# Kernel tuning notes

Measured on AMD Instinct MI355X. Metric: run time of the kernel, lower is better.

## Reference

```python
import jax, jax.numpy as jnp
import numpy as np

HIDDEN = 100  # hard-coded in the torch module


def setup_inputs() -> dict:
    key = jax.random.key(0)
    k1, k2, k3, k4, k5 = jax.random.split(key, 5)
    dims, N, M = 32, 4096, 8192
    centroids = jax.random.normal(k1, (N, dims), dtype=jnp.float32)
    x = jax.random.normal(k2, (M, dims), dtype=jnp.float32)
    # torch Linear params: y = x @ W.T (+ b)
    W1 = jax.random.normal(k3, (HIDDEN, dims), dtype=jnp.float32) / np.sqrt(dims)
    W2 = jax.random.normal(k4, (dims, HIDDEN), dtype=jnp.float32) / np.sqrt(HIDDEN)
    b2 = jax.random.uniform(k5, (dims,), dtype=jnp.float32, minval=-0.1, maxval=0.1)
    return {"centroids": centroids, "x": x, "W1": W1, "W2": W2, "b2": b2}


def reference(centroids, x, W1, W2, b2):
    dims = centroids.shape[1]
    # small MLP: Linear(dims,100,no bias) -> Linear(100,dims) -> tanh, then gate by centroids
    loc = jnp.tanh((centroids @ W1.T) @ W2.T + b2) * centroids  # [N, dims]
    # covariance = eye(dims) * var(centroids) (scalar, unbiased var over all elements)
    var = jnp.var(centroids, ddof=1)
    # diagonal-Gaussian log_prob, pairwise [N, M] via ||x-loc||^2 expansion (no NxMxD cube)
    sq = (
        jnp.sum(x * x, axis=1)[None, :]
        + jnp.sum(loc * loc, axis=1)[:, None]
        - 2.0 * (loc @ x.T)
    )  # [N, M]
    log_norm = dims * jnp.log(2.0 * jnp.pi * var)
    logp = -0.5 * (sq / var + log_norm)  # [N, M]
    return jnp.exp(logp).T  # [M, N]
```

## Files before the change

kernel.cpp:

```cpp
#include <hip/hip_runtime.h>
#include <math.h>

#define DIMS 32
#define NROWS 4096
#define MROWS 8192
#define HID 100

#define L2E 1.44269504088896340736f

typedef float f32x4 __attribute__((ext_vector_type(4)));
typedef short bf16x8 __attribute__((ext_vector_type(8)));

__global__ __launch_bounds__(256) void k_init(const float* __restrict__ c,
                                              const float* __restrict__ W1,
                                              const float* __restrict__ W2,
                                              float* __restrict__ part,
                                              float* __restrict__ Mmat) {
    int b = blockIdx.x, t = threadIdx.x;
    const float4* c4 = (const float4*)c;
    float s = 0.0f, q = 0.0f;
    #pragma unroll
    for (int i = 0; i < 16; i++) {
        float4 a = c4[b * 4096 + i * 256 + t];
        s += a.x + a.y + a.z + a.w;
        q += a.x * a.x + a.y * a.y + a.z * a.z + a.w * a.w;
    }
    #pragma unroll
    for (int off = 32; off > 0; off >>= 1) {
        s += __shfl_down(s, off);
        q += __shfl_down(q, off);
    }
    __shared__ float red[8];
    int lane = t & 63, wid = t >> 6;
    if (lane == 0) { red[wid] = s; red[4 + wid] = q; }
    __syncthreads();
    if (t == 0) {
        part[2 * b]     = red[0] + red[1] + red[2] + red[3];
        part[2 * b + 1] = red[4] + red[5] + red[6] + red[7];
    }
    if (b == 0) {
        __shared__ float w1s[HID * DIMS];
        __shared__ float w2s[DIMS * HID];
        for (int i = t; i < HID * DIMS; i += 256) { w1s[i] = W1[i]; w2s[i] = W2[i]; }
        __syncthreads();
        #pragma unroll
        for (int o = 0; o < 4; o++) {
            int id = o * 256 + t;
            int r = id >> 5, cc = id & 31;
            float a = 0.0f;
            for (int j = 0; j < HID; j++) a += w2s[r * HID + j] * w1s[j * DIMS + cc];
            Mmat[id] = a;
        }
    }
}

__device__ __forceinline__ void load_var(const float* part, float& iv, float& var) {
    float S = 0.0f, Q = 0.0f;
    #pragma unroll
    for (int i = 0; i < 8; i++) { S += part[2 * i]; Q += part[2 * i + 1]; }
    const float cnt = (float)(NROWS * DIMS);
    var = (Q - S * S / cnt) / (cnt - 1.0f);
    iv = 1.0f / var;
}

__device__ __forceinline__ float tanh_fast(float x) {
    float xc = fminf(fmaxf(x, -10.0f), 10.0f);
    float e = __builtin_amdgcn_exp2f(xc * (2.0f * L2E));
    return (e - 1.0f) * __builtin_amdgcn_rcpf(e + 1.0f);
}

__device__ __forceinline__ unsigned short f2bf(float f) {
    unsigned int u = __float_as_uint(f);
    u += 0x7FFFu + ((u >> 16) & 1u);
    return (unsigned short)(u >> 16);
}

__global__ __launch_bounds__(256) void k_prep(const float* __restrict__ cent,
                                              const float* __restrict__ x,
                                              const float* __restrict__ b2,
                                              const float* __restrict__ part,
                                              const float* __restrict__ Mmat,
                                              float* __restrict__ A,
                                              float* __restrict__ B,
                                              unsigned short* __restrict__ xb,
                                              unsigned short* __restrict__ locb) {
    float iv, var;
    load_var(part, iv, var);
    const float hv = -0.5f * L2E * iv;
    int t = threadIdx.x;

    if (blockIdx.x < 16) {
        __shared__ __align__(16) float ms[DIMS * DIMS];
        __shared__ float b2s[DIMS];
        for (int i = t; i < DIMS * DIMS; i += 256) ms[i] = Mmat[i];
        if (t < DIMS) b2s[t] = b2[t];
        __syncthreads();

        int n = blockIdx.x * 256 + t;
        float c[DIMS];
        const float4* cr = (const float4*)(cent + (size_t)n * DIMS);
        #pragma unroll
        for (int i = 0; i < 8; i++) {
            float4 v = cr[i];
            c[4 * i] = v.x; c[4 * i + 1] = v.y; c[4 * i + 2] = v.z; c[4 * i + 3] = v.w;
        }
        float lr[DIMS];
        float lsq = 0.0f;
        #pragma unroll
        for (int d = 0; d < DIMS; d++) {
            const float4* mr = (const float4*)&ms[d * DIMS];
            float a0 = 0.f, a1 = 0.f, a2 = 0.f, a3 = 0.f;
            #pragma unroll
            for (int kk = 0; kk < 8; kk++) {
                float4 m = mr[kk];
                a0 += c[4 * kk] * m.x;
                a1 += c[4 * kk + 1] * m.y;
                a2 += c[4 * kk + 2] * m.z;
                a3 += c[4 * kk + 3] * m.w;
            }
            float v = tanh_fast((a0 + a1) + (a2 + a3) + b2s[d]) * c[d];
            lr[d] = v;
            lsq += v * v;
        }
        unsigned int w[16];
        #pragma unroll
        for (int d = 0; d < 16; d++)
            w[d] = (unsigned int)f2bf(lr[2 * d]) | ((unsigned int)f2bf(lr[2 * d + 1]) << 16);
        uint4* lo = (uint4*)(locb + (size_t)n * DIMS);
        lo[0] = make_uint4(w[0], w[1], w[2], w[3]);
        lo[1] = make_uint4(w[4], w[5], w[6], w[7]);
        lo[2] = make_uint4(w[8], w[9], w[10], w[11]);
        lo[3] = make_uint4(w[12], w[13], w[14], w[15]);
        B[n] = hv * lsq;
    } else {
        int m = (blockIdx.x - 16) * 256 + t;
        const float4* xr = (const float4*)(x + (size_t)m * DIMS);
        float xsq = 0.0f;
        unsigned int w[16];
        #pragma unroll
        for (int i = 0; i < 8; i++) {
            float4 v = xr[i];
            xsq += v.x * v.x + v.y * v.y + v.z * v.z + v.w * v.w;
            w[2 * i]     = (unsigned int)f2bf(v.x) | ((unsigned int)f2bf(v.y) << 16);
            w[2 * i + 1] = (unsigned int)f2bf(v.z) | ((unsigned int)f2bf(v.w) << 16);
        }
        uint4* xo = (uint4*)(xb + (size_t)m * DIMS);
        xo[0] = make_uint4(w[0], w[1], w[2], w[3]);
        xo[1] = make_uint4(w[4], w[5], w[6], w[7]);
        xo[2] = make_uint4(w[8], w[9], w[10], w[11]);
        xo[3] = make_uint4(w[12], w[13], w[14], w[15]);
        float C0 = -16.0f * log2f(2.0f * (float)M_PI * var);
        A[m] = hv * xsq + C0;
    }
}

__global__ __launch_bounds__(256) void k_pair(const unsigned short* __restrict__ xb,
                                              const unsigned short* __restrict__ locb,
                                              const float* __restrict__ A,
                                              const float* __restrict__ B,
                                              const float* __restrict__ part,
                                              float* __restrict__ out) {
    float iv, var;
    load_var(part, iv, var);
    const float s = L2E * iv;

    int t = threadIdx.x;
    int lane = t & 63, wid = t >> 6;
    int m0 = blockIdx.y * 128 + (wid >> 1) * 64;
    int n0 = blockIdx.x * 128 + (wid & 1) * 64;
    int r = lane & 15, g = lane >> 4;

    bf16x8 af[4], bfr[4];
    #pragma unroll
    for (int i = 0; i < 4; i++)
        af[i] = *(const bf16x8*)(xb + (size_t)(m0 + 16 * i + r) * DIMS + 8 * g);
    #pragma unroll
    for (int j = 0; j < 4; j++)
        bfr[j] = *(const bf16x8*)(locb + (size_t)(n0 + 16 * j + r) * DIMS + 8 * g);

    f32x4 zero = {0.0f, 0.0f, 0.0f, 0.0f};
    f32x4 acc[4][4];
    #pragma unroll
    for (int i = 0; i < 4; i++)
        #pragma unroll
        for (int j = 0; j < 4; j++)
            acc[i][j] = __builtin_amdgcn_mfma_f32_16x16x32_bf16(af[i], bfr[j], zero, 0, 0, 0);

    float Av[4][4];
    #pragma unroll
    for (int i = 0; i < 4; i++)
        #pragma unroll
        for (int q = 0; q < 4; q++)
            Av[i][q] = A[m0 + 16 * i + 4 * g + q];
    float Bv[4];
    #pragma unroll
    for (int j = 0; j < 4; j++)
        Bv[j] = B[n0 + 16 * j + r];

    #pragma unroll
    for (int i = 0; i < 4; i++) {
        #pragma unroll
        for (int q = 0; q < 4; q++) {
            float* orow = out + (size_t)(m0 + 16 * i + 4 * g + q) * NROWS + n0 + r;
            float aq = Av[i][q];
            #pragma unroll
            for (int j = 0; j < 4; j++) {
                float v = __builtin_amdgcn_exp2f(fmaf(s, acc[i][j][q], aq + Bv[j]));
                __builtin_nontemporal_store(v, orow + 16 * j);
            }
        }
    }
}

extern "C" void kernel_launch(void* const* d_in, const int* in_sizes, int n_in,
                              void* d_out, int out_size, void* d_ws, size_t ws_size,
                              hipStream_t stream) {
    const float* cent = (const float*)d_in[0];
    const float* x    = (const float*)d_in[1];
    const float* W1   = (const float*)d_in[2];
    const float* W2   = (const float*)d_in[3];
    const float* b2   = (const float*)d_in[4];
    float* out = (float*)d_out;

    float* ws   = (float*)d_ws;
    float* part = ws;
    float* Mmat = ws + 64;
    float* A    = Mmat + 1024;
    float* B    = A + MROWS;
    unsigned short* xb   = (unsigned short*)(B + NROWS);
    unsigned short* locb = xb + (size_t)MROWS * DIMS;

    k_init<<<8, 256, 0, stream>>>(cent, W1, W2, part, Mmat);
    k_prep<<<48, 256, 0, stream>>>(cent, x, b2, part, Mmat, A, B, xb, locb);
    k_pair<<<dim3(NROWS / 128, MROWS / 128), 256, 0, stream>>>(xb, locb, A, B, part, out);
}
```

Measured before the change: 178.3 us.

## Merge init into prep, transpose MFMA operands for vector stores, swizzle tiles

Folds the variance partial-sum kernel into the prep kernel. Each loc block now recomputes the 32x32 W2·W1 product itself, and the variance scaling moves into the pair kernel, which removes one launch and the dependency between the two small kernels. The pair kernel swaps the MFMA operand order so each lane holds four consecutive output columns. That allows 16-byte nontemporal stores in place of scalar ones. Block indices are also remapped with an XCD-aware swizzle. The cost is redundant 32x32x100 matmul work in 16 blocks.

```diff
diff --git a/kernel.cpp b/kernel.cpp
--- a/kernel.cpp
+++ b/kernel.cpp
@@ -11,37 +11,68 @@
 typedef float f32x4 __attribute__((ext_vector_type(4)));
 typedef short bf16x8 __attribute__((ext_vector_type(8)));
 
-__global__ __launch_bounds__(256) void k_init(const float* __restrict__ c,
+__device__ __forceinline__ void load_var(const float* part, float& iv, float& var) {
+    float S = 0.0f, Q = 0.0f;
+    #pragma unroll
+    for (int i = 0; i < 8; i++) { S += part[2 * i]; Q += part[2 * i + 1]; }
+    const float cnt = (float)(NROWS * DIMS);
+    var = (Q - S * S / cnt) / (cnt - 1.0f);
+    iv = 1.0f / var;
+}
+
+__device__ __forceinline__ float tanh_fast(float x) {
+    float xc = fminf(fmaxf(x, -10.0f), 10.0f);
+    float e = __builtin_amdgcn_exp2f(xc * (2.0f * L2E));
+    return (e - 1.0f) * __builtin_amdgcn_rcpf(e + 1.0f);
+}
+
+__device__ __forceinline__ unsigned short f2bf(float f) {
+    unsigned int u = __float_as_uint(f);
+    u += 0x7FFFu + ((u >> 16) & 1u);
+    return (unsigned short)(u >> 16);
+}
+
+__global__ __launch_bounds__(256) void k_prep(const float* __restrict__ cent,
+                                              const float* __restrict__ x,
                                               const float* __restrict__ W1,
                                               const float* __restrict__ W2,
+                                              const float* __restrict__ b2,
                                               float* __restrict__ part,
-                                              float* __restrict__ Mmat) {
+                                              float* __restrict__ A,
+                                              float* __restrict__ B,
+                                              unsigned short* __restrict__ xb,
+                                              unsigned short* __restrict__ locb) {
     int b = blockIdx.x, t = threadIdx.x;
-    const float4* c4 = (const float4*)c;
-    float s = 0.0f, q = 0.0f;
-    #pragma unroll
-    for (int i = 0; i < 16; i++) {
-        float4 a = c4[b * 4096 + i * 256 + t];
-        s += a.x + a.y + a.z + a.w;
-        q += a.x * a.x + a.y * a.y + a.z * a.z + a.w * a.w;
-    }
-    #pragma unroll
-    for (int off = 32; off > 0; off >>= 1) {
-        s += __shfl_down(s, off);
-        q += __shfl_down(q, off);
-    }
-    __shared__ float red[8];
-    int lane = t & 63, wid = t >> 6;
-    if (lane == 0) { red[wid] = s; red[4 + wid] = q; }
-    __syncthreads();
-    if (t == 0) {
-        part[2 * b]     = red[0] + red[1] + red[2] + red[3];
-        part[2 * b + 1] = red[4] + red[5] + red[6] + red[7];
-    }
-    if (b == 0) {
+
+    if (b < 8) {
+        const float4* c4 = (const float4*)cent;
+        float s = 0.0f, q = 0.0f;
+        #pragma unroll
+        for (int i = 0; i < 16; i++) {
+            float4 a = c4[b * 4096 + i * 256 + t];
+            s += a.x + a.y + a.z + a.w;
+            q += a.x * a.x + a.y * a.y + a.z * a.z + a.w * a.w;
+        }
+        #pragma unroll
+        for (int off = 32; off > 0; off >>= 1) {
+            s += __shfl_down(s, off);
+            q += __shfl_down(q, off);
+        }
+        __shared__ float red[8];
+        int lane = t & 63, wid = t >> 6;
+        if (lane == 0) { red[wid] = s; red[4 + wid] = q; }
+        __syncthreads();
+        if (t == 0) {
+            part[2 * b]     = red[0] + red[1] + red[2] + red[3];
+            part[2 * b + 1] = red[4] + red[5] + red[6] + red[7];
+        }
+    } else if (b < 24) {
         __shared__ float w1s[HID * DIMS];
         __shared__ float w2s[DIMS * HID];
+        __shared__ __align__(16) float ms[DIMS * DIMS];
+        __shared__ float b2s[DIMS];
         for (int i = t; i < HID * DIMS; i += 256) { w1s[i] = W1[i]; w2s[i] = W2[i]; }
+        if (t < DIMS) b2s[t] = b2[t];
         __syncthreads();
         #pragma unroll
         for (int o = 0; o < 4; o++) {
@@ -49,54 +80,11 @@
             int r = id >> 5, cc = id & 31;
             float a = 0.0f;
             for (int j = 0; j < HID; j++) a += w2s[r * HID + j] * w1s[j * DIMS + cc];
-            Mmat[id] = a;
-        }
-    }
-}
-
-__device__ __forceinline__ void load_var(const float* part, float& iv, float& var) {
-    float S = 0.0f, Q = 0.0f;
-    #pragma unroll
-    for (int i = 0; i < 8; i++) { S += part[2 * i]; Q += part[2 * i + 1]; }
-    const float cnt = (float)(NROWS * DIMS);
-    var = (Q - S * S / cnt) / (cnt - 1.0f);
-    iv = 1.0f / var;
-}
-
-__device__ __forceinline__ float tanh_fast(float x) {
-    float xc = fminf(fmaxf(x, -10.0f), 10.0f);
-    float e = __builtin_amdgcn_exp2f(xc * (2.0f * L2E));
-    return (e - 1.0f) * __builtin_amdgcn_rcpf(e + 1.0f);
-}
-
-__device__ __forceinline__ unsigned short f2bf(float f) {
-    unsigned int u = __float_as_uint(f);
-    u += 0x7FFFu + ((u >> 16) & 1u);
-    return (unsigned short)(u >> 16);
-}
-
-__global__ __launch_bounds__(256) void k_prep(const float* __restrict__ cent,
-                                              const float* __restrict__ x,
-                                              const float* __restrict__ b2,
-                                              const float* __restrict__ part,
-                                              const float* __restrict__ Mmat,
-                                              float* __restrict__ A,
-                                              float* __restrict__ B,
-                                              unsigned short* __restrict__ xb,
-                                              unsigned short* __restrict__ locb) {
-    float iv, var;
-    load_var(part, iv, var);
-    const float hv = -0.5f * L2E * iv;
-    int t = threadIdx.x;
-
-    if (blockIdx.x < 16) {
-        __shared__ __align__(16) float ms[DIMS * DIMS];
-        __shared__ float b2s[DIMS];
-        for (int i = t; i < DIMS * DIMS; i += 256) ms[i] = Mmat[i];
-        if (t < DIMS) b2s[t] = b2[t];
+            ms[id] = a;
+        }
         __syncthreads();
 
-        int n = blockIdx.x * 256 + t;
+        int n = (b - 8) * 256 + t;
         float c[DIMS];
         const float4* cr = (const float4*)(cent + (size_t)n * DIMS);
         #pragma unroll
@@ -131,9 +119,9 @@
         lo[1] = make_uint4(w[4], w[5], w[6], w[7]);
         lo[2] = make_uint4(w[8], w[9], w[10], w[11]);
         lo[3] = make_uint4(w[12], w[13], w[14], w[15]);
-        B[n] = hv * lsq;
+        B[n] = lsq;
     } else {
-        int m = (blockIdx.x - 16) * 256 + t;
+        int m = (b - 24) * 256 + t;
         const float4* xr = (const float4*)(x + (size_t)m * DIMS);
         float xsq = 0.0f;
         unsigned int w[16];
@@ -149,8 +137,7 @@
         xo[1] = make_uint4(w[4], w[5], w[6], w[7]);
         xo[2] = make_uint4(w[8], w[9], w[10], w[11]);
         xo[3] = make_uint4(w[12], w[13], w[14], w[15]);
-        float C0 = -16.0f * log2f(2.0f * (float)M_PI * var);
-        A[m] = hv * xsq + C0;
+        A[m] = xsq;
     }
 }
 
@@ -162,52 +149,58 @@
                                               float* __restrict__ out) {
     float iv, var;
     load_var(part, iv, var);
-    const float s = L2E * iv;
+    const float s  = L2E * iv;
+    const float hv = -0.5f * L2E * iv;
+    const float C0 = -16.0f * log2f(2.0f * (float)M_PI * var);
 
     int t = threadIdx.x;
     int lane = t & 63, wid = t >> 6;
-    int m0 = blockIdx.y * 128 + (wid >> 1) * 64;
-    int n0 = blockIdx.x * 128 + (wid & 1) * 64;
+    int bid = blockIdx.x;
+    int tile = ((bid & 7) << 8) | (bid >> 3);
+    int mt = tile >> 5, ntl = tile & 31;
+    int m0 = mt * 128 + (wid >> 1) * 64;
+    int n0 = ntl * 128 + (wid & 1) * 64;
     int r = lane & 15, g = lane >> 4;
 
-    bf16x8 af[4], bfr[4];
+    bf16x8 lf[4], xf[4];
+    #pragma unroll
+    for (int j = 0; j < 4; j++)
+        lf[j] = *(const bf16x8*)(locb + (size_t)(n0 + 16 * j + r) * DIMS + 8 * g);
     #pragma unroll
     for (int i = 0; i < 4; i++)
-        af[i] = *(const bf16x8*)(xb + (size_t)(m0 + 16 * i + r) * DIMS + 8 * g);
-    #pragma unroll
-    for (int j = 0; j < 4; j++)
-        bfr[j] = *(const bf16x8*)(locb + (size_t)(n0 + 16 * j + r) * DIMS + 8 * g);
+        xf[i] = *(const bf16x8*)(xb + (size_t)(m0 + 16 * i + r) * DIMS + 8 * g);
 
     f32x4 zero = {0.0f, 0.0f, 0.0f, 0.0f};
     f32x4 acc[4][4];
     #pragma unroll
+    for (int j = 0; j < 4; j++)
+        #pragma unroll
+        for (int i = 0; i < 4; i++)
+            acc[j][i] = __builtin_amdgcn_mfma_f32_16x16x32_bf16(lf[j], xf[i], zero, 0, 0, 0);
+
+    float em[4];
+    #pragma unroll
     for (int i = 0; i < 4; i++)
-        #pragma unroll
-        for (int j = 0; j < 4; j++)
-            acc[i][j] = __builtin_amdgcn_mfma_f32_16x16x32_bf16(af[i], bfr[j], zero, 0, 0, 0);
-
-    float Av[4][4];
-    #pragma unroll
-    for (int i = 0; i < 4; i++)
-        #pragma unroll
-        for (int q = 0; q < 4; q++)
-            Av[i][q] = A[m0 + 16 * i + 4 * g + q];
-    float Bv[4];
-    #pragma unroll
-    for (int j = 0; j < 4; j++)
-        Bv[j] = B[n0 + 16 * j + r];
+        em[i] = fmaf(hv, A[m0 + 16 * i + r], C0);
+    f32x4 en[4];
+    #pragma unroll
+    for (int j = 0; j < 4; j++) {
+        float4 bv = *(const float4*)&B[n0 + 16 * j + 4 * g];
+        en[j].x = hv * bv.x; en[j].y = hv * bv.y; en[j].z = hv * bv.z; en[j].w = hv * bv.w;
+    }
 
     #pragma unroll
     for (int i = 0; i < 4; i++) {
-        #pragma unroll
-        for (int q = 0; q < 4; q++) {
-            float* orow = out + (size_t)(m0 + 16 * i + 4 * g + q) * NROWS + n0 + r;
-            float aq = Av[i][q];
-            #pragma unroll
-            for (int j = 0; j < 4; j++) {
-                float v = __builtin_amdgcn_exp2f(fmaf(s, acc[i][j][q], aq + Bv[j]));
-                __builtin_nontemporal_store(v, orow + 16 * j);
-            }
+        float* orow = out + (size_t)(m0 + 16 * i + r) * NROWS;
+        float e = em[i];
+        #pragma unroll
+        for (int j = 0; j < 4; j++) {
+            f32x4 v;
+            v.x = __builtin_amdgcn_exp2f(fmaf(s, acc[j][i][0], e + en[j].x));
+            v.y = __builtin_amdgcn_exp2f(fmaf(s, acc[j][i][1], e + en[j].y));
+            v.z = __builtin_amdgcn_exp2f(fmaf(s, acc[j][i][2], e + en[j].z));
+            v.w = __builtin_amdgcn_exp2f(fmaf(s, acc[j][i][3], e + en[j].w));
+            __builtin_nontemporal_store(v, (f32x4*)(orow + n0 + 16 * j + 4 * g));
         }
     }
 }
@@ -224,13 +217,11 @@
 
     float* ws   = (float*)d_ws;
     float* part = ws;
-    float* Mmat = ws + 64;
-    float* A    = Mmat + 1024;
+    float* A    = ws + 64;
     float* B    = A + MROWS;
     unsigned short* xb   = (unsigned short*)(B + NROWS);
     unsigned short* locb = xb + (size_t)MROWS * DIMS;
 
-    k_init<<<8, 256, 0, stream>>>(cent, W1, W2, part, Mmat);
-    k_prep<<<48, 256, 0, stream>>>(cent, x, b2, part, Mmat, A, B, xb, locb);
-    k_pair<<<dim3(NROWS / 128, MROWS / 128), 256, 0, stream>>>(xb, locb, A, B, part, out);
-}
+    k_prep<<<56, 256, 0, stream>>>(cent, x, W1, W2, b2, part, A, B, xb, locb);
+    k_pair<<<NROWS / 128 * (MROWS / 128), 256, 0, stream>>>(xb, locb, A, B, part, out);
+}
```

Measured after the change: 176.2 us. Within noise of the previous version (-1.2%).
